# Optimization experiments

Hardware: AMD Instinct MI355X
Metric: run time of the kernel (lower is better)

The kernel has to match this reference:

```python
import jax, jax.numpy as jnp
import numpy as np
from jax import lax

S_INIT = 0.025
ALPHA = 0.98
DELTA = 2.0
R = 0.5
EPS = 1e-6


def setup_inputs() -> dict:
    key = jax.random.key(0)
    k1, _ = jax.random.split(key)
    B, F, T = 32, 128, 8000
    x = jax.random.uniform(k1, (B, F, T), dtype=jnp.float32)  # nonneg mel energies
    log_s = jnp.full((F,), np.log(S_INIT), dtype=jnp.float32)
    return {"x": x, "log_s": log_s}


def _pcen(x, log_s):
    # x: (B, F, T) or (B, C, F, T)
    squeeze = False
    if x.ndim == 3:
        x = x[:, None]  # (B, 1, F, T)
        squeeze = True
    s = jnp.exp(log_s)[None, None, :]  # (1, 1, F), broadcasts over (B, C, F)
    xt = jnp.moveaxis(x, -1, 0)  # (T, B, C, F)
    m0 = xt[0]

    def step(m_prev, x_i):
        m = (1.0 - s) * m_prev + s * x_i
        return m, m

    _, ms = lax.scan(step, m0, xt[1:])  # (T-1, B, C, F)
    M = jnp.concatenate([m0[None], ms], axis=0)  # (T, B, C, F)
    M = jnp.moveaxis(M, 0, -1)  # (B, C, F, T)
    out = (x / (EPS + M) ** ALPHA + DELTA) ** R - DELTA ** R
    return out[:, 0] if squeeze else out.squeeze(1)


def reference(x, log_s):
    return _pcen(x, log_s)
```

## Files before the change

kernel.cpp:

```cpp
#include <hip/hip_runtime.h>


#define T_LEN 8000
#define F_DIM 128
#define NSEQ  4096
#define HALO_ITERS 3

typedef __attribute__((ext_vector_type(4))) float vfloat4;

__device__ __forceinline__ float hw_log2(float v) { return __builtin_amdgcn_logf(v); }
__device__ __forceinline__ float hw_exp2(float v) { return __builtin_amdgcn_exp2f(v); }

__device__ __forceinline__ float pcen_out(float xi, float m) {
    float p = hw_exp2(-0.98f * hw_log2(1e-6f + m));
    return __builtin_amdgcn_sqrtf(fmaf(xi, p, 2.0f)) - 1.4142135623730951f;
}

template<int CTRL, int RMASK>
__device__ __forceinline__ float dpp0(float v) {
    return __int_as_float(__builtin_amdgcn_update_dpp(
        0, __float_as_int(v), CTRL, RMASK, 0xF, true));
}

__device__ __forceinline__ float wscan64(float P, float dk1, float dk2, float dk4,
                                         float dk8, float w15, float w31) {
    P = fmaf(dk1, dpp0<0x111, 0xF>(P), P);
    P = fmaf(dk2, dpp0<0x112, 0xF>(P), P);
    P = fmaf(dk4, dpp0<0x114, 0xF>(P), P);
    P = fmaf(dk8, dpp0<0x118, 0xF>(P), P);
    P = fmaf(w15, dpp0<0x142, 0xA>(P), P);
    P = fmaf(w31, dpp0<0x143, 0xC>(P), P);
    return P;
}

__global__ __launch_bounds__(256, 4) void pcen_kernel(const float* __restrict__ x,
                                                      const float* __restrict__ log_s,
                                                      float* __restrict__ out) {
    const int lane  = threadIdx.x & 63;
    const int wid   = blockIdx.x * 4 + (threadIdx.x >> 6);
    const int seq   = wid >> 2;
    const int chunk = wid & 3;
    const int f     = seq & (F_DIM - 1);

    const float* xp = x   + (size_t)seq * T_LEN;
    float*       op = out + (size_t)seq * T_LEN;

    const int halo = (chunk == 0) ? 0 : HALO_ITERS;
    const int S    = (chunk == 0) ? 0 : 2560 + (chunk - 1) * 1792;
    const int base = S - halo * 256;

    const float4* xv4 = (const float4*)(xp + base);
    vfloat4*      ov4 = (vfloat4*)(op + base);

    float4 r0 = xv4[0 * 64 + lane];
    float4 r1 = xv4[1 * 64 + lane];
    float4 r2 = xv4[2 * 64 + lane];
    float4 r3 = xv4[3 * 64 + lane];
    float4 r4 = xv4[4 * 64 + lane];
    float4 r5 = xv4[5 * 64 + lane];
    float4 r6 = xv4[6 * 64 + lane];
    float4 r7 = xv4[7 * 64 + lane];
    float4 r8 = xv4[8 * 64 + lane];
    float4 r9 = xv4[9 * 64 + lane];
    float  x0 = xp[0];
    float  xt = 0.0f;
    if (chunk == 3) xt = xp[7936 + lane];
    __builtin_amdgcn_sched_barrier(0);

    const float s   = hw_exp2(log_s[f] * 1.4426950408889634f);
    const float a   = 1.0f - s;
    const float l2a = hw_log2(a);

    const float a2 = a * a;
    const float a3 = a2 * a;
    const float a4 = a2 * a2;
    const float c0 = a4;
    const float c1 = c0 * c0;
    const float c2 = c1 * c1;
    const float c3 = c2 * c2;
    const float c4 = c3 * c3;
    const float c5 = c4 * c4;
    const float a256 = c5 * c5;
    const float a4l = hw_exp2((float)(4 * lane) * l2a);
    const float inv_a4 = 1.0f / a4;
    const float w15 = hw_exp2((float)(4 * ((lane & 15) + 1)) * l2a);
    const float w31 = hw_exp2((float)(4 * ((lane & 31) + 1)) * l2a);

    float carry = (chunk == 0) ? x0 : 0.0f;

#define PCEN_IT(xv, kk)                                                        \
    {                                                                          \
        float B0 = s * xv.x;                                                   \
        float B1 = fmaf(a, B0, s * xv.y);                                      \
        float B2 = fmaf(a, B1, s * xv.z);                                      \
        float B3 = fmaf(a, B2, s * xv.w);                                      \
        float P  = wscan64(B3, c0, c1, c2, c3, w15, w31);                      \
        float E  = (P - B3) * inv_a4;                                          \
        float C  = fmaf(a4l, carry, E);                                        \
        float P63 = __int_as_float(                                            \
            __builtin_amdgcn_readlane(__float_as_int(P), 63));                 \
        carry = fmaf(a256, carry, P63);                                        \
        if ((kk) >= halo) {                                  \
            float m0 = fmaf(a,  C, B0);                                        \
            float m1 = fmaf(a2, C, B1);                                        \
            float m2 = fmaf(a3, C, B2);                                        \
            float m3 = fmaf(a4, C, B3);                                        \
            vfloat4 o;                                                         \
            o.x = pcen_out(xv.x, m0);                                          \
            o.y = pcen_out(xv.y, m1);                                          \
            o.z = pcen_out(xv.z, m2);                                          \
            o.w = pcen_out(xv.w, m3);                                          \
            __builtin_nontemporal_store(o, &ov4[(kk) * 64 + lane]);            \
        }                                                                      \
    }

    PCEN_IT(r0, 0)
    PCEN_IT(r1, 1)
    PCEN_IT(r2, 2)
    PCEN_IT(r3, 3)
    PCEN_IT(r4, 4)
    PCEN_IT(r5, 5)
    PCEN_IT(r6, 6)
    PCEN_IT(r7, 7)
    PCEN_IT(r8, 8)
    PCEN_IT(r9, 9)
#undef PCEN_IT

    if (chunk == 3) {
        const float al1  = hw_exp2((float)(lane + 1) * l2a);
        const float w15t = hw_exp2((float)((lane & 15) + 1) * l2a);
        const float w31t = hw_exp2((float)((lane & 31) + 1) * l2a);
        float P = wscan64(s * xt, a, a2, a4, c1, w15t, w31t);
        float m = fmaf(al1, carry, P);
        op[7936 + lane] = pcen_out(xt, m);
    }
}

extern "C" void kernel_launch(void* const* d_in, const int* in_sizes, int n_in,
                              void* d_out, int out_size, void* d_ws, size_t ws_size,
                              hipStream_t stream) {
    const float* x     = (const float*)d_in[0];
    const float* log_s = (const float*)d_in[1];
    float*       out   = (float*)d_out;
    pcen_kernel<<<dim3(NSEQ), dim3(256), 0, stream>>>(x, log_s, out);
}
```

Before: 225.4 us.

## Shrink halo to two iterations and use nontemporal loads

Cuts the warm-up halo for non-first chunks from three 256-sample iterations to two, so those chunks now handle nine iterations instead of ten, and only chunk 0 loads and processes the tenth. Input loads become nontemporal, log_s is read before the x loads, and the initial carry comes from a readlane of r0 instead of a separate scalar load of x[0]. This removes redundant memory traffic and recurrence work. The risk is accuracy: a shorter halo leaves a larger decayed-carry error at chunk starts, since a^512 with s=0.025 is about 2.4e-6, which is small but relies on s not being tiny.

```diff
diff --git a/kernel.cpp b/kernel.cpp
--- a/kernel.cpp
+++ b/kernel.cpp
@@ -4,7 +4,7 @@
 #define T_LEN 8000
 #define F_DIM 128
 #define NSEQ  4096
-#define HALO_ITERS 3
+#define HALO_ITERS 2
 
 typedef __attribute__((ext_vector_type(4))) float vfloat4;
 
@@ -45,29 +45,31 @@
     const float* xp = x   + (size_t)seq * T_LEN;
     float*       op = out + (size_t)seq * T_LEN;
 
+    const float ls = log_s[f];
+
     const int halo = (chunk == 0) ? 0 : HALO_ITERS;
     const int S    = (chunk == 0) ? 0 : 2560 + (chunk - 1) * 1792;
     const int base = S - halo * 256;
 
-    const float4* xv4 = (const float4*)(xp + base);
-    vfloat4*      ov4 = (vfloat4*)(op + base);
+    const vfloat4* xv4 = (const vfloat4*)(xp + base);
+    vfloat4*       ov4 = (vfloat4*)(op + base);
 
-    float4 r0 = xv4[0 * 64 + lane];
-    float4 r1 = xv4[1 * 64 + lane];
-    float4 r2 = xv4[2 * 64 + lane];
-    float4 r3 = xv4[3 * 64 + lane];
-    float4 r4 = xv4[4 * 64 + lane];
-    float4 r5 = xv4[5 * 64 + lane];
-    float4 r6 = xv4[6 * 64 + lane];
-    float4 r7 = xv4[7 * 64 + lane];
-    float4 r8 = xv4[8 * 64 + lane];
-    float4 r9 = xv4[9 * 64 + lane];
-    float  x0 = xp[0];
-    float  xt = 0.0f;
-    if (chunk == 3) xt = xp[7936 + lane];
+    vfloat4 r0 = __builtin_nontemporal_load(&xv4[0 * 64 + lane]);
+    vfloat4 r1 = __builtin_nontemporal_load(&xv4[1 * 64 + lane]);
+    vfloat4 r2 = __builtin_nontemporal_load(&xv4[2 * 64 + lane]);
+    vfloat4 r3 = __builtin_nontemporal_load(&xv4[3 * 64 + lane]);
+    vfloat4 r4 = __builtin_nontemporal_load(&xv4[4 * 64 + lane]);
+    vfloat4 r5 = __builtin_nontemporal_load(&xv4[5 * 64 + lane]);
+    vfloat4 r6 = __builtin_nontemporal_load(&xv4[6 * 64 + lane]);
+    vfloat4 r7 = __builtin_nontemporal_load(&xv4[7 * 64 + lane]);
+    vfloat4 r8 = __builtin_nontemporal_load(&xv4[8 * 64 + lane]);
+    vfloat4 r9 = {0.0f, 0.0f, 0.0f, 0.0f};
+    if (chunk == 0) r9 = __builtin_nontemporal_load(&xv4[9 * 64 + lane]);
+    float xt = 0.0f;
+    if (chunk == 3) xt = __builtin_nontemporal_load(xp + 7936 + lane);
     __builtin_amdgcn_sched_barrier(0);
 
-    const float s   = hw_exp2(log_s[f] * 1.4426950408889634f);
+    const float s   = hw_exp2(ls * 1.4426950408889634f);
     const float a   = 1.0f - s;
     const float l2a = hw_log2(a);
 
@@ -86,7 +88,9 @@
     const float w15 = hw_exp2((float)(4 * ((lane & 15) + 1)) * l2a);
     const float w31 = hw_exp2((float)(4 * ((lane & 31) + 1)) * l2a);
 
-    float carry = (chunk == 0) ? x0 : 0.0f;
+    float carry = (chunk == 0)
+        ? __int_as_float(__builtin_amdgcn_readlane(__float_as_int(r0.x), 0))
+        : 0.0f;
 
 #define PCEN_IT(xv, kk)                                                        \
     {                                                                          \
@@ -123,7 +127,7 @@
     PCEN_IT(r6, 6)
     PCEN_IT(r7, 7)
     PCEN_IT(r8, 8)
-    PCEN_IT(r9, 9)
+    if (chunk == 0) PCEN_IT(r9, 9)
 #undef PCEN_IT
 
     if (chunk == 3) {
```

After: 218.0 us. 1.03x faster.
